# Optimization experiments

Hardware: AMD Instinct MI355X
Metric: run time of the kernel (lower is better)

## Reference

```python
import jax, jax.numpy as jnp
import numpy as np

N = 50000   # nodes
E = 800000  # edges
D = 128     # input feature dim
H = 128     # hidden_channels
O = 128     # out_channels
NEG_SLOPE = 0.2


def setup_inputs() -> dict:
    key = jax.random.key(0)
    ks = jax.random.split(key, 16)
    x = jax.random.normal(ks[0], (N, D), dtype=jnp.float32)
    edge_idx = jax.random.randint(ks[1], (2, E), 0, N, dtype=jnp.int32)

    def lin(k, fin, fout):
        return jax.random.normal(k, (fin, fout), dtype=jnp.float32) / np.sqrt(fin)

    params = {
        # layer 1 (D -> H)
        "Wl1": lin(ks[2], D, H), "bl1": jnp.zeros((H,), jnp.float32),
        "Wr1": lin(ks[3], D, H), "br1": jnp.zeros((H,), jnp.float32),
        "att1": jax.random.normal(ks[4], (H,), dtype=jnp.float32) / np.sqrt(H),
        "b1": jnp.zeros((H,), jnp.float32),
        # layer 2 (H -> O)
        "Wl2": lin(ks[5], H, O), "bl2": jnp.zeros((O,), jnp.float32),
        "Wr2": lin(ks[6], H, O), "br2": jnp.zeros((O,), jnp.float32),
        "att2": jax.random.normal(ks[7], (O,), dtype=jnp.float32) / np.sqrt(O),
        "b2": jnp.zeros((O,), jnp.float32),
    }
    return {"x": x, "edge_idx": edge_idx, **params}


def gatv2_layer(x, src, dst, Wl, bl, Wr, br, att, bias):
    """Single-head GATv2Conv (add_self_loops=False), PyG semantics.

    message(x_j) uses lin_l(x_j); score uses leaky_relu(lin_l(x_j)+lin_r(x_i)) @ att,
    softmax over in-edges of each target node, scatter-add weighted messages.
    """
    xl = x @ Wl + bl            # [N, F] source transform
    xr = x @ Wr + br            # [N, F] target transform
    msg = xl[src]               # [E, F] gathered source messages
    e = jax.nn.leaky_relu(msg + xr[dst], NEG_SLOPE)  # [E, F]
    s = e @ att                 # [E] unnormalized scores
    smax = jax.lax.stop_gradient(jax.ops.segment_max(s, dst, num_segments=N))
    p = jnp.exp(s - smax[dst])  # stable segment softmax numerator
    denom = jax.ops.segment_sum(p, dst, num_segments=N)  # [N]
    alpha = p / denom[dst]      # [E]
    out = jax.ops.segment_sum(alpha[:, None] * msg, dst, num_segments=N)
    return out + bias


def reference(x, edge_idx, Wl1, bl1, Wr1, br1, att1, b1, Wl2, bl2, Wr2, br2, att2, b2):
    src, dst = edge_idx[0], edge_idx[1]
    h = jax.nn.relu(gatv2_layer(x, src, dst, Wl1, bl1, Wr1, br1, att1, b1))
    out = gatv2_layer(h, src, dst, Wl2, bl2, Wr2, br2, att2, b2)
    return out
```

## Files before the change

### kernel.cpp

```cpp
#include <hip/hip_runtime.h>
#include <math.h>


typedef short bf16x8 __attribute__((ext_vector_type(8)));
typedef float f32x4 __attribute__((ext_vector_type(4)));

#define LDK 136
#define SMEM_BYTES (2 * 32 * LDK * 2)

__global__ __launch_bounds__(256) void prep_zero_kernel(
    const float* __restrict__ W0, const float* __restrict__ W1,
    const float* __restrict__ W2, const float* __restrict__ W3,
    short* __restrict__ wt, int* __restrict__ deg8, int total8N) {
    int b = blockIdx.x;
    for (int j = b * 256 + threadIdx.x; j < total8N; j += 32 * 256) deg8[j] = 0;
    int mat = b >> 3, chunk = b & 7;
    const float* W = (mat == 0) ? W0 : (mat == 1) ? W1 : (mat == 2) ? W2 : W3;
    short* hi = wt + (size_t)mat * 2 * 16384;
    short* lo = hi + 16384;
    int i0 = chunk * 2048;
    for (int i = i0 + threadIdx.x; i < i0 + 2048; i += 256) {
        int k = i >> 7, n = i & 127;
        float x = W[i];
        unsigned u = __float_as_uint(x);
        unsigned hu = u & 0xFFFF0000u;
        float lf = x - __uint_as_float(hu);
        hi[n * 128 + k] = (short)(hu >> 16);
        lo[n * 128 + k] = (short)(__float_as_uint(lf) >> 16);
    }
}

__device__ __forceinline__ void gemm_dual32_body(
    int bx, const float* __restrict__ X, const short* __restrict__ wtL,
    const float* __restrict__ b0, short* __restrict__ out0bf,
    const float* __restrict__ b1, float* __restrict__ out1,
    int Nrows, char* smem) {
    short (*Ahi)[LDK] = (short (*)[LDK])smem;
    short (*Alo)[LDK] = (short (*)[LDK])(smem + 32 * LDK * 2);

    int tid = threadIdx.x;
    int w = tid >> 6, lane = tid & 63, q = lane >> 4, tr = lane & 15;
    int m0 = bx * 32;
    int n0 = w * 32;

    bf16x8 bh[4], bl[4];
    #pragma unroll
    for (int p = 0; p < 2; ++p) {
        const short* base = wtL + (size_t)p * 2 * 16384;
        #pragma unroll
        for (int nt = 0; nt < 2; ++nt) {
            size_t boff = (size_t)(n0 + nt * 16 + tr) * 128 + q * 8;
            bh[p * 2 + nt] = *(const bf16x8*)&base[boff];
            bl[p * 2 + nt] = *(const bf16x8*)&base[16384 + boff];
        }
    }

    {
        int srow = tid >> 3;
        int c0 = (tid & 7) * 16;
        int gr = m0 + srow; if (gr >= Nrows) gr = Nrows - 1;
        const float* xp = &X[(size_t)gr * 128 + c0];
        float4 v[4];
        #pragma unroll
        for (int j = 0; j < 4; ++j) v[j] = *(const float4*)(xp + j * 4);
        #pragma unroll
        for (int j = 0; j < 2; ++j) {
            bf16x8 hv, lv;
            #pragma unroll
            for (int k = 0; k < 2; ++k) {
                float4 vv = v[j * 2 + k];
                float f[4] = {vv.x, vv.y, vv.z, vv.w};
                #pragma unroll
                for (int e = 0; e < 4; ++e) {
                    unsigned u = __float_as_uint(f[e]);
                    unsigned hu = u & 0xFFFF0000u;
                    float lf = f[e] - __uint_as_float(hu);
                    hv[k * 4 + e] = (short)(hu >> 16);
                    lv[k * 4 + e] = (short)(__float_as_uint(lf) >> 16);
                }
            }
            *(bf16x8*)&Ahi[srow][c0 + j * 8] = hv;
            *(bf16x8*)&Alo[srow][c0 + j * 8] = lv;
        }
    }
    __syncthreads();

    f32x4 acc[2][4];
    #pragma unroll
    for (int a = 0; a < 2; ++a)
        #pragma unroll
        for (int b = 0; b < 4; ++b) acc[a][b] = (f32x4){0.f, 0.f, 0.f, 0.f};

    for (int kc = 0; kc < 128; kc += 32) {
        #pragma unroll
        for (int mt = 0; mt < 2; ++mt) {
            bf16x8 ah = *(const bf16x8*)&Ahi[mt * 16 + tr][kc + q * 8];
            bf16x8 al = *(const bf16x8*)&Alo[mt * 16 + tr][kc + q * 8];
            #pragma unroll
            for (int j = 0; j < 4; ++j) {
                acc[mt][j] = __builtin_amdgcn_mfma_f32_16x16x32_bf16(ah, bh[j], acc[mt][j], 0, 0, 0);
                acc[mt][j] = __builtin_amdgcn_mfma_f32_16x16x32_bf16(ah, bl[j], acc[mt][j], 0, 0, 0);
                acc[mt][j] = __builtin_amdgcn_mfma_f32_16x16x32_bf16(al, bh[j], acc[mt][j], 0, 0, 0);
            }
        }
        if (kc < 96) {
            #pragma unroll
            for (int p = 0; p < 2; ++p) {
                const short* base = wtL + (size_t)p * 2 * 16384;
                #pragma unroll
                for (int nt = 0; nt < 2; ++nt) {
                    size_t boff = (size_t)(n0 + nt * 16 + tr) * 128 + (kc + 32) + q * 8;
                    bh[p * 2 + nt] = *(const bf16x8*)&base[boff];
                    bl[p * 2 + nt] = *(const bf16x8*)&base[16384 + boff];
                }
            }
        }
    }

    int orow = tid >> 3;
    int oc0 = (tid & 7) * 16;
    int gr = m0 + orow;

    float (*Ofp)[132] = (float (*)[132])smem;
    __syncthreads();
    #pragma unroll
    for (int nt = 0; nt < 2; ++nt) {
        float bv1 = b1[n0 + nt * 16 + tr];
        #pragma unroll
        for (int mt = 0; mt < 2; ++mt)
            #pragma unroll
            for (int r = 0; r < 4; ++r)
                Ofp[mt * 16 + q * 4 + r][n0 + nt * 16 + tr] = acc[mt][2 + nt][r] + bv1;
    }
    __syncthreads();
    if (gr < Nrows) {
        #pragma unroll
        for (int j = 0; j < 4; ++j)
            *(float4*)&out1[(size_t)gr * 128 + oc0 + j * 4] = *(float4*)&Ofp[orow][oc0 + j * 4];
    }
    __syncthreads();

    short (*Obf)[136] = (short (*)[136])smem;
    #pragma unroll
    for (int nt = 0; nt < 2; ++nt) {
        float bv0 = b0[n0 + nt * 16 + tr];
        #pragma unroll
        for (int mt = 0; mt < 2; ++mt)
            #pragma unroll
            for (int r = 0; r < 4; ++r) {
                float v0 = acc[mt][nt][r] + bv0;
                unsigned u = __float_as_uint(v0);
                unsigned rb = (u + 0x7FFFu + ((u >> 16) & 1u)) >> 16;
                Obf[mt * 16 + q * 4 + r][n0 + nt * 16 + tr] = (short)rb;
            }
    }
    __syncthreads();
    if (gr < Nrows) {
        *(bf16x8*)&out0bf[(size_t)gr * 128 + oc0]     = *(bf16x8*)&Obf[orow][oc0];
        *(bf16x8*)&out0bf[(size_t)gr * 128 + oc0 + 8] = *(bf16x8*)&Obf[orow][oc0 + 8];
    }
}

__global__ __launch_bounds__(256) void gemm_mfma_dual32_kernel(
    const float* __restrict__ X, const short* __restrict__ wtL,
    const float* __restrict__ b0, short* __restrict__ out0bf,
    const float* __restrict__ b1, float* __restrict__ out1, int Nrows) {
    __shared__ __attribute__((aligned(16))) char smem[SMEM_BYTES];
    gemm_dual32_body(blockIdx.x, X, wtL, b0, out0bf, b1, out1, Nrows, smem);
}

__global__ __launch_bounds__(256) void gemm1_count_kernel(
    const float* __restrict__ X, const short* __restrict__ wtL,
    const float* __restrict__ b0, short* __restrict__ out0bf,
    const float* __restrict__ b1, float* __restrict__ out1,
    int Nrows, int gemmBlocks,
    const int* __restrict__ dst, int* __restrict__ deg8,
    unsigned short* __restrict__ rank16, int E, int N) {
    __shared__ __attribute__((aligned(16))) char smem[SMEM_BYTES];
    int bx = blockIdx.x;
    int base3 = 3 * gemmBlocks;
    int cb;
    if (bx < base3) {
        int role = bx % 3, g = bx / 3;
        if (role == 0) {
            gemm_dual32_body(g, X, wtL, b0, out0bf, b1, out1, Nrows, smem);
            return;
        }
        cb = g * 2 + (role - 1);
    } else {
        cb = 2 * gemmBlocks + (bx - base3);
    }
    int i = cb * 256 + threadIdx.x;
    if (i < E) {
        int slice = (i >> 8) & 7;
        int r = atomicAdd(&deg8[(size_t)slice * N + dst[i]], 1);
        rank16[i] = (unsigned short)r;
    }
}

__global__ __launch_bounds__(256) void scan_blocksum2_kernel(
    const int* __restrict__ deg8, unsigned short* __restrict__ base8,
    int* __restrict__ dtot, int* __restrict__ blockSums, int n) {
    __shared__ int wsum[4];
    int tid = threadIdx.x;
    int idx = blockIdx.x * 256 + tid;
    int lane = tid & 63, wid = tid >> 6;
    int tot = 0;
    if (idx < n) {
        int b = 0;
        #pragma unroll
        for (int s = 0; s < 8; ++s) {
            int v = deg8[(size_t)s * n + idx];
            base8[(size_t)s * n + idx] = (unsigned short)b;
            b += v;
        }
        tot = b;
        dtot[idx] = tot;
    }
    int v = tot;
    #pragma unroll
    for (int off = 32; off > 0; off >>= 1) v += __shfl_xor(v, off);
    if (lane == 0) wsum[wid] = v;
    __syncthreads();
    if (tid == 0) blockSums[blockIdx.x] = wsum[0] + wsum[1] + wsum[2] + wsum[3];
}

__global__ __launch_bounds__(256) void scan_apply2_kernel(
    const int* __restrict__ dtot, const int* __restrict__ blockSums,
    const unsigned short* __restrict__ base8,
    int* __restrict__ row_ptr, int* __restrict__ rpb, int n, int nBlk) {
    __shared__ int sPre[4], sAll[4], wsum[4];
    int tid = threadIdx.x, lane = tid & 63, wid = tid >> 6;

    int bsv = (tid < nBlk) ? blockSums[tid] : 0;
    int pre = (tid < (int)blockIdx.x) ? bsv : 0;
    int all = bsv;
    #pragma unroll
    for (int off = 32; off > 0; off >>= 1) {
        pre += __shfl_xor(pre, off);
        all += __shfl_xor(all, off);
    }
    if (lane == 0) { sPre[wid] = pre; sAll[wid] = all; }
    __syncthreads();
    int off0 = sPre[0] + sPre[1] + sPre[2] + sPre[3];
    int total = sAll[0] + sAll[1] + sAll[2] + sAll[3];

    int idx = blockIdx.x * 256 + tid;
    int v = (idx < n) ? dtot[idx] : 0;
    int incl = v;
    #pragma unroll
    for (int off = 1; off < 64; off <<= 1) {
        int t = __shfl_up(incl, off);
        if (lane >= off) incl += t;
    }
    if (lane == 63) wsum[wid] = incl;
    __syncthreads();
    int woff = 0;
    #pragma unroll
    for (int w = 0; w < 4; ++w) woff += (w < wid) ? wsum[w] : 0;
    int excl = off0 + woff + (incl - v);
    if (idx < n) {
        row_ptr[idx] = excl;
        #pragma unroll
        for (int s = 0; s < 8; ++s)
            rpb[(size_t)s * n + idx] = excl + (int)base8[(size_t)s * n + idx];
    }
    if (blockIdx.x == 0 && tid == 0) row_ptr[n] = total;
}

__global__ void scatter_edges_kernel(const int* __restrict__ src, const int* __restrict__ dst,
                                     const int* __restrict__ rpb,
                                     const unsigned short* __restrict__ rank16,
                                     unsigned short* __restrict__ csr16, int E, int N) {
    int i = blockIdx.x * blockDim.x + threadIdx.x;
    if (i < E) {
        int d = dst[i];
        int slice = (i >> 8) & 7;
        int pos = rpb[(size_t)slice * N + d] + (int)rank16[i];
        csr16[pos] = (unsigned short)src[i];
    }
}

__global__ __launch_bounds__(256) void gat_aggregate_kernel(
    const short* __restrict__ xl16, const float* __restrict__ xr,
    const float* __restrict__ att, const float* __restrict__ bias,
    const int* __restrict__ row_ptr, const unsigned short* __restrict__ csr16,
    float* __restrict__ out, int N, int applyRelu) {
    int wid = threadIdx.x >> 6;
    int lane = threadIdx.x & 63;
    int qlane = lane & 15;
    int qid = lane >> 4;
    int node = blockIdx.x * 4 + wid;
    if (node >= N) return;

    const bf16x8* xlb = (const bf16x8*)xl16;
    float4 xrA = ((const float4*)xr)[(size_t)node * 32 + qlane * 2];
    float4 xrB = ((const float4*)xr)[(size_t)node * 32 + qlane * 2 + 1];
    float4 atA = ((const float4*)att)[qlane * 2];
    float4 atB = ((const float4*)att)[qlane * 2 + 1];

    int beg = row_ptr[node];
    int end = row_ptr[node + 1];

    float dsum = 0.f;
    float4 accA = {0.f, 0.f, 0.f, 0.f};
    float4 accB = {0.f, 0.f, 0.f, 0.f};

    for (int cbase = beg; cbase < end; cbase += 64) {
        int cnt = end - cbase;
        if (cnt > 64) cnt = 64;
        int myidx = (lane < cnt) ? (int)csr16[cbase + lane] : 0;
        int nq = (cnt + 3) >> 2;

        for (int g = 0; g < nq; ++g) {
            int eidx = 4 * g + qid;
            int s = __shfl(myidx, eidx);
            bf16x8 mv = xlb[((size_t)s << 4) + qlane];
            float4 vA, vB;
            vA.x = __uint_as_float(((unsigned)(unsigned short)mv[0]) << 16);
            vA.y = __uint_as_float(((unsigned)(unsigned short)mv[1]) << 16);
            vA.z = __uint_as_float(((unsigned)(unsigned short)mv[2]) << 16);
            vA.w = __uint_as_float(((unsigned)(unsigned short)mv[3]) << 16);
            vB.x = __uint_as_float(((unsigned)(unsigned short)mv[4]) << 16);
            vB.y = __uint_as_float(((unsigned)(unsigned short)mv[5]) << 16);
            vB.z = __uint_as_float(((unsigned)(unsigned short)mv[6]) << 16);
            vB.w = __uint_as_float(((unsigned)(unsigned short)mv[7]) << 16);

            float t, p;
            t = vA.x + xrA.x; t = fmaxf(t, 0.2f * t); p = t * atA.x;
            t = vA.y + xrA.y; t = fmaxf(t, 0.2f * t); p = fmaf(t, atA.y, p);
            t = vA.z + xrA.z; t = fmaxf(t, 0.2f * t); p = fmaf(t, atA.z, p);
            t = vA.w + xrA.w; t = fmaxf(t, 0.2f * t); p = fmaf(t, atA.w, p);
            t = vB.x + xrB.x; t = fmaxf(t, 0.2f * t); p = fmaf(t, atB.x, p);
            t = vB.y + xrB.y; t = fmaxf(t, 0.2f * t); p = fmaf(t, atB.y, p);
            t = vB.z + xrB.z; t = fmaxf(t, 0.2f * t); p = fmaf(t, atB.z, p);
            t = vB.w + xrB.w; t = fmaxf(t, 0.2f * t); p = fmaf(t, atB.w, p);

            p += __shfl_xor(p, 1);
            p += __shfl_xor(p, 2);
            p += __shfl_xor(p, 4);
            p += __shfl_xor(p, 8);

            float e = (eidx < cnt) ? __expf(p) : 0.f;
            dsum += e;
            accA.x = fmaf(e, vA.x, accA.x);
            accA.y = fmaf(e, vA.y, accA.y);
            accA.z = fmaf(e, vA.z, accA.z);
            accA.w = fmaf(e, vA.w, accA.w);
            accB.x = fmaf(e, vB.x, accB.x);
            accB.y = fmaf(e, vB.y, accB.y);
            accB.z = fmaf(e, vB.z, accB.z);
            accB.w = fmaf(e, vB.w, accB.w);
        }
    }

    #pragma unroll
    for (int off = 16; off <= 32; off <<= 1) {
        dsum += __shfl_xor(dsum, off);
        accA.x += __shfl_xor(accA.x, off);
        accA.y += __shfl_xor(accA.y, off);
        accA.z += __shfl_xor(accA.z, off);
        accA.w += __shfl_xor(accA.w, off);
        accB.x += __shfl_xor(accB.x, off);
        accB.y += __shfl_xor(accB.y, off);
        accB.z += __shfl_xor(accB.z, off);
        accB.w += __shfl_xor(accB.w, off);
    }

    float inv = dsum > 0.f ? 1.f / dsum : 0.f;
    float4 bvA = ((const float4*)bias)[qlane * 2];
    float4 bvB = ((const float4*)bias)[qlane * 2 + 1];
    float4 oA, oB;
    oA.x = accA.x * inv + bvA.x; oA.y = accA.y * inv + bvA.y;
    oA.z = accA.z * inv + bvA.z; oA.w = accA.w * inv + bvA.w;
    oB.x = accB.x * inv + bvB.x; oB.y = accB.y * inv + bvB.y;
    oB.z = accB.z * inv + bvB.z; oB.w = accB.w * inv + bvB.w;
    if (applyRelu) {
        oA.x = fmaxf(oA.x, 0.f); oA.y = fmaxf(oA.y, 0.f);
        oA.z = fmaxf(oA.z, 0.f); oA.w = fmaxf(oA.w, 0.f);
        oB.x = fmaxf(oB.x, 0.f); oB.y = fmaxf(oB.y, 0.f);
        oB.z = fmaxf(oB.z, 0.f); oB.w = fmaxf(oB.w, 0.f);
    }
    if (lane < 16) {
        ((float4*)out)[(size_t)node * 32 + qlane * 2] = oA;
        ((float4*)out)[(size_t)node * 32 + qlane * 2 + 1] = oB;
    }
}


extern "C" void kernel_launch(void* const* d_in, const int* in_sizes, int n_in,
                              void* d_out, int out_size, void* d_ws, size_t ws_size,
                              hipStream_t stream) {
    const float* x    = (const float*)d_in[0];
    const int* eidx   = (const int*)d_in[1];
    const float* Wl1  = (const float*)d_in[2];
    const float* bl1  = (const float*)d_in[3];
    const float* Wr1  = (const float*)d_in[4];
    const float* br1  = (const float*)d_in[5];
    const float* att1 = (const float*)d_in[6];
    const float* b1   = (const float*)d_in[7];
    const float* Wl2  = (const float*)d_in[8];
    const float* bl2  = (const float*)d_in[9];
    const float* Wr2  = (const float*)d_in[10];
    const float* br2  = (const float*)d_in[11];
    const float* att2 = (const float*)d_in[12];
    const float* b2   = (const float*)d_in[13];

    const int N = in_sizes[0] / 128;
    const int E = in_sizes[1] / 2;
    const int* src = eidx;
    const int* dst = eidx + E;

    const int nBlk = (N + 255) / 256;

    size_t NF = (size_t)N * 128;
    short* xl16 = (short*)d_ws;
    float* bufB = (float*)(xl16 + NF);
    float* bufC = bufB + NF;
    int* deg8      = (int*)(bufC + NF);
    int* dtot      = deg8 + 8 * (size_t)N;
    int* row_ptr   = dtot + N;
    int* blockSums = row_ptr + (N + 1);
    int* rpb       = blockSums + nBlk;
    unsigned short* base8  = (unsigned short*)(rpb + 8 * (size_t)N);
    unsigned short* rank16 = base8 + 8 * (size_t)N;
    unsigned short* csr16  = rank16 + E;
    short* wt      = (short*)(csr16 + E);

    float* outF = (float*)d_out;

    const int nCnt = (E + 255) / 256;
    const int gemmBlocks = (N + 31) / 32;
    int fusedGrid = 3 * gemmBlocks;
    if (nCnt > 2 * gemmBlocks) fusedGrid += nCnt - 2 * gemmBlocks;
    dim3 aggGrid((N + 3) / 4);

    prep_zero_kernel<<<32, 256, 0, stream>>>(Wl1, Wr1, Wl2, Wr2, wt, deg8, 8 * N);
    gemm1_count_kernel<<<fusedGrid, 256, 0, stream>>>(
        x, wt, bl1, xl16, br1, bufB, N, gemmBlocks, dst, deg8, rank16, E, N);
    scan_blocksum2_kernel<<<nBlk, 256, 0, stream>>>(deg8, base8, dtot, blockSums, N);
    scan_apply2_kernel<<<nBlk, 256, 0, stream>>>(dtot, blockSums, base8, row_ptr, rpb, N, nBlk);
    scatter_edges_kernel<<<nCnt, 256, 0, stream>>>(src, dst, rpb, rank16, csr16, E, N);
    gat_aggregate_kernel<<<aggGrid, 256, 0, stream>>>(xl16, bufB, att1, b1, row_ptr, csr16,
                                                      bufC, N, 1);
    gemm_mfma_dual32_kernel<<<gemmBlocks, 256, 0, stream>>>(bufC, wt + 2 * 2 * 16384, bl2, xl16,
                                                            br2, bufB, N);
    gat_aggregate_kernel<<<aggGrid, 256, 0, stream>>>(xl16, bufB, att2, b2, row_ptr, csr16,
                                                      outF, N, 0);
}
```

Baseline: 286.3 us.

## Fuse two-pass prefix scan into single kernel with decoupled block-sum publishing

Measured after the change: 284.5 us. Within noise of the previous version (-0.6%).

```diff
diff --git a/kernel.cpp b/kernel.cpp
--- a/kernel.cpp
+++ b/kernel.cpp
@@ -11,9 +11,9 @@
 __global__ __launch_bounds__(256) void prep_zero_kernel(
     const float* __restrict__ W0, const float* __restrict__ W1,
     const float* __restrict__ W2, const float* __restrict__ W3,
-    short* __restrict__ wt, int* __restrict__ deg8, int total8N) {
+    short* __restrict__ wt, int* __restrict__ zbase, int ztotal) {
     int b = blockIdx.x;
-    for (int j = b * 256 + threadIdx.x; j < total8N; j += 32 * 256) deg8[j] = 0;
+    for (int j = b * 256 + threadIdx.x; j < ztotal; j += 32 * 256) zbase[j] = 0;
     int mat = b >> 3, chunk = b & 7;
     const float* W = (mat == 0) ? W0 : (mat == 1) ? W1 : (mat == 2) ? W2 : W3;
     short* hi = wt + (size_t)mat * 2 * 16384;
@@ -198,74 +198,69 @@
     }
 }
 
-__global__ __launch_bounds__(256) void scan_blocksum2_kernel(
-    const int* __restrict__ deg8, unsigned short* __restrict__ base8,
-    int* __restrict__ dtot, int* __restrict__ blockSums, int n) {
-    __shared__ int wsum[4];
-    int tid = threadIdx.x;
+__global__ __launch_bounds__(256) void scan_fused_kernel(
+    const int* __restrict__ deg8, int* __restrict__ pub,
+    int* __restrict__ row_ptr, int* __restrict__ rpb, int n, int nBlk) {
+    __shared__ int sA[4], sB[4];
+    __shared__ int sBsum;
+    int tid = threadIdx.x, lane = tid & 63, wid = tid >> 6;
     int idx = blockIdx.x * 256 + tid;
-    int lane = tid & 63, wid = tid >> 6;
+
+    int b8[8];
     int tot = 0;
     if (idx < n) {
-        int b = 0;
         #pragma unroll
         for (int s = 0; s < 8; ++s) {
             int v = deg8[(size_t)s * n + idx];
-            base8[(size_t)s * n + idx] = (unsigned short)b;
-            b += v;
-        }
-        tot = b;
-        dtot[idx] = tot;
-    }
+            b8[s] = tot;
+            tot += v;
+        }
+    }
+
     int v = tot;
     #pragma unroll
     for (int off = 32; off > 0; off >>= 1) v += __shfl_xor(v, off);
-    if (lane == 0) wsum[wid] = v;
-    __syncthreads();
-    if (tid == 0) blockSums[blockIdx.x] = wsum[0] + wsum[1] + wsum[2] + wsum[3];
-}
-
-__global__ __launch_bounds__(256) void scan_apply2_kernel(
-    const int* __restrict__ dtot, const int* __restrict__ blockSums,
-    const unsigned short* __restrict__ base8,
-    int* __restrict__ row_ptr, int* __restrict__ rpb, int n, int nBlk) {
-    __shared__ int sPre[4], sAll[4], wsum[4];
-    int tid = threadIdx.x, lane = tid & 63, wid = tid >> 6;
-
-    int bsv = (tid < nBlk) ? blockSums[tid] : 0;
-    int pre = (tid < (int)blockIdx.x) ? bsv : 0;
-    int all = bsv;
-    #pragma unroll
-    for (int off = 32; off > 0; off >>= 1) {
-        pre += __shfl_xor(pre, off);
-        all += __shfl_xor(all, off);
-    }
-    if (lane == 0) { sPre[wid] = pre; sAll[wid] = all; }
-    __syncthreads();
-    int off0 = sPre[0] + sPre[1] + sPre[2] + sPre[3];
-    int total = sAll[0] + sAll[1] + sAll[2] + sAll[3];
-
-    int idx = blockIdx.x * 256 + tid;
-    int v = (idx < n) ? dtot[idx] : 0;
-    int incl = v;
+    if (lane == 0) sA[wid] = v;
+    __syncthreads();
+    if (tid == 0) {
+        int bs = sA[0] + sA[1] + sA[2] + sA[3];
+        sBsum = bs;
+        atomicExch(&pub[blockIdx.x], bs + 1);
+    }
+    __syncthreads();
+    int bsum = sBsum;
+
+    int pv = 0;
+    if (tid < (int)blockIdx.x) {
+        while ((pv = atomicAdd(&pub[tid], 0)) == 0) {}
+        pv -= 1;
+    }
+    int pr = pv;
+    #pragma unroll
+    for (int off = 32; off > 0; off >>= 1) pr += __shfl_xor(pr, off);
+    if (lane == 0) sB[wid] = pr;
+    __syncthreads();
+    int off0 = sB[0] + sB[1] + sB[2] + sB[3];
+
+    int incl = tot;
     #pragma unroll
     for (int off = 1; off < 64; off <<= 1) {
         int t = __shfl_up(incl, off);
         if (lane >= off) incl += t;
     }
-    if (lane == 63) wsum[wid] = incl;
+    if (lane == 63) sA[wid] = incl;
     __syncthreads();
     int woff = 0;
     #pragma unroll
-    for (int w = 0; w < 4; ++w) woff += (w < wid) ? wsum[w] : 0;
-    int excl = off0 + woff + (incl - v);
+    for (int w = 0; w < 4; ++w) woff += (w < wid) ? sA[w] : 0;
+    int excl = off0 + woff + (incl - tot);
     if (idx < n) {
         row_ptr[idx] = excl;
         #pragma unroll
         for (int s = 0; s < 8; ++s)
-            rpb[(size_t)s * n + idx] = excl + (int)base8[(size_t)s * n + idx];
-    }
-    if (blockIdx.x == 0 && tid == 0) row_ptr[n] = total;
+            rpb[(size_t)s * n + idx] = excl + b8[s];
+    }
+    if ((int)blockIdx.x == nBlk - 1 && tid == 0) row_ptr[n] = off0 + bsum;
 }
 
 __global__ void scatter_edges_kernel(const int* __restrict__ src, const int* __restrict__ dst,
@@ -293,7 +288,7 @@
     int node = blockIdx.x * 4 + wid;
     if (node >= N) return;
 
-    const bf16x8* xlb = (const bf16x8*)xl16;
+    const uint4* xlb = (const uint4*)xl16;
     float4 xrA = ((const float4*)xr)[(size_t)node * 32 + qlane * 2];
     float4 xrB = ((const float4*)xr)[(size_t)node * 32 + qlane * 2 + 1];
     float4 atA = ((const float4*)att)[qlane * 2];
@@ -315,16 +310,16 @@
         for (int g = 0; g < nq; ++g) {
             int eidx = 4 * g + qid;
             int s = __shfl(myidx, eidx);
-            bf16x8 mv = xlb[((size_t)s << 4) + qlane];
+            uint4 md = xlb[((size_t)s << 4) + qlane];
             float4 vA, vB;
-            vA.x = __uint_as_float(((unsigned)(unsigned short)mv[0]) << 16);
-            vA.y = __uint_as_float(((unsigned)(unsigned short)mv[1]) << 16);
-            vA.z = __uint_as_float(((unsigned)(unsigned short)mv[2]) << 16);
-            vA.w = __uint_as_float(((unsigned)(unsigned short)mv[3]) << 16);
-            vB.x = __uint_as_float(((unsigned)(unsigned short)mv[4]) << 16);
-            vB.y = __uint_as_float(((unsigned)(unsigned short)mv[5]) << 16);
-            vB.z = __uint_as_float(((unsigned)(unsigned short)mv[6]) << 16);
-            vB.w = __uint_as_float(((unsigned)(unsigned short)mv[7]) << 16);
+            vA.x = __uint_as_float(md.x << 16);
+            vA.y = __uint_as_float(md.x & 0xFFFF0000u);
+            vA.z = __uint_as_float(md.y << 16);
+            vA.w = __uint_as_float(md.y & 0xFFFF0000u);
+            vB.x = __uint_as_float(md.z << 16);
+            vB.y = __uint_as_float(md.z & 0xFFFF0000u);
+            vB.z = __uint_as_float(md.w << 16);
+            vB.w = __uint_as_float(md.w & 0xFFFF0000u);
 
             float t, p;
             t = vA.x + xrA.x; t = fmaxf(t, 0.2f * t); p = t * atA.x;
@@ -418,12 +413,10 @@
     float* bufB = (float*)(xl16 + NF);
     float* bufC = bufB + NF;
     int* deg8      = (int*)(bufC + NF);
-    int* dtot      = deg8 + 8 * (size_t)N;
-    int* row_ptr   = dtot + N;
-    int* blockSums = row_ptr + (N + 1);
-    int* rpb       = blockSums + nBlk;
-    unsigned short* base8  = (unsigned short*)(rpb + 8 * (size_t)N);
-    unsigned short* rank16 = base8 + 8 * (size_t)N;
+    int* pub       = deg8 + 8 * (size_t)N;
+    int* row_ptr   = pub + nBlk;
+    int* rpb       = row_ptr + (N + 1);
+    unsigned short* rank16 = (unsigned short*)(rpb + 8 * (size_t)N);
     unsigned short* csr16  = rank16 + E;
     short* wt      = (short*)(csr16 + E);
 
@@ -435,11 +428,10 @@
     if (nCnt > 2 * gemmBlocks) fusedGrid += nCnt - 2 * gemmBlocks;
     dim3 aggGrid((N + 3) / 4);
 
-    prep_zero_kernel<<<32, 256, 0, stream>>>(Wl1, Wr1, Wl2, Wr2, wt, deg8, 8 * N);
+    prep_zero_kernel<<<32, 256, 0, stream>>>(Wl1, Wr1, Wl2, Wr2, wt, deg8, 8 * N + nBlk);
     gemm1_count_kernel<<<fusedGrid, 256, 0, stream>>>(
         x, wt, bl1, xl16, br1, bufB, N, gemmBlocks, dst, deg8, rank16, E, N);
-    scan_blocksum2_kernel<<<nBlk, 256, 0, stream>>>(deg8, base8, dtot, blockSums, N);
-    scan_apply2_kernel<<<nBlk, 256, 0, stream>>>(dtot, blockSums, base8, row_ptr, rpb, N, nBlk);
+    scan_fused_kernel<<<nBlk, 256, 0, stream>>>(deg8, pub, row_ptr, rpb, N, nBlk);
     scatter_edges_kernel<<<nCnt, 256, 0, stream>>>(src, dst, rpb, rank16, csr16, E, N);
     gat_aggregate_kernel<<<aggGrid, 256, 0, stream>>>(xl16, bufB, att1, b1, row_ptr, csr16,
                                                       bufC, N, 1);
```
